# Kernel tuning notes

Measured on AMD Instinct MI355X. Metric: run time of the kernel, lower is better.

The kernel has to match this reference:

```python
import jax, jax.numpy as jnp
import numpy as np

B, S, H = 2, 2048, 1024
NH = 16
HD = H // NH


def setup_inputs() -> dict:
    key = jax.random.key(0)
    ks = jax.random.split(key, 5)
    X = jax.random.normal(ks[0], (B, S, H), dtype=jnp.float32)
    mask = jnp.ones((B, S), dtype=jnp.int32)
    W_Q = jax.random.normal(ks[1], (H, H), dtype=jnp.float32) * 0.02
    W_K = jax.random.normal(ks[2], (H, H), dtype=jnp.float32) * 0.02
    W_V = jax.random.normal(ks[3], (H, H), dtype=jnp.float32) * 0.02
    W_O = jax.random.normal(ks[4], (H, H), dtype=jnp.float32) * 0.02
    return {"X": X, "mask": mask, "W_Q": W_Q, "W_K": W_K, "W_V": W_V, "W_O": W_O}


def reference(X, mask, W_Q, W_K, W_V, W_O):
    b, s, h = X.shape
    scaling = HD ** -0.5
    # project and split heads: [b, nh, s, hd]
    Q = (X @ W_Q).reshape(b, s, NH, HD).transpose(0, 2, 1, 3)
    K = (X @ W_K).reshape(b, s, NH, HD).transpose(0, 2, 1, 3)
    V = (X @ W_V).reshape(b, s, NH, HD).transpose(0, 2, 1, 3)
    scores = jnp.einsum('bhqd,bhkd->bhqk', Q, K) * scaling
    scores = jnp.clip(scores, -10000.0, 10000.0)
    # 2D mask [b, s] -> broadcast as [b, 1, 1, s]; fill -inf where mask == 0
    m = mask[:, None, None, :]
    scores = jnp.where(m == 0, -jnp.inf, scores)
    attn = jax.nn.softmax(scores, axis=-1)
    # dropout is identity in eval / p=0
    context = jnp.einsum('bhqk,bhkd->bhqd', attn, V)
    context = context.transpose(0, 2, 1, 3).reshape(b, s, h)
    return context @ W_O
```

## Files before the change

### kernel.cpp

```cpp
#include <hip/hip_runtime.h>
#include <hip/hip_bf16.h>

#define S_LEN 2048
#define HDIM  1024
#define NHEADS 16
#define HD    64
#define QKV_STRIDE (S_LEN * 2 * HDIM)

typedef __attribute__((ext_vector_type(8))) short short8;
typedef __attribute__((ext_vector_type(4))) float float4v;

__device__ __forceinline__ unsigned short f2bf(float f) {
  return (unsigned short)((__builtin_bit_cast(unsigned int, f) + 0x8000u) >> 16);
}
__device__ __forceinline__ unsigned int pkbf(float a, float b) {
  unsigned int ua = __builtin_bit_cast(unsigned int, a) + 0x8000u;
  unsigned int ub = __builtin_bit_cast(unsigned int, b) + 0x8000u;
  return __builtin_amdgcn_perm(ub, ua, 0x07060302u);
}

__device__ __forceinline__ void async_copy16(const void* g, void* l) {
  __builtin_amdgcn_global_load_lds((__attribute__((address_space(1))) const void*)g,
                                   (__attribute__((address_space(3))) void*)l, 16, 0, 0);
}

__global__ void cast_x_kernel(const float* __restrict__ X, unsigned short* __restrict__ Xb) {
  int i = blockIdx.x * blockDim.x + threadIdx.x;
  float4 v = ((const float4*)X)[i];
  uint2 o;
  o.x = pkbf(v.x, v.y);
  o.y = pkbf(v.z, v.w);
  ((uint2*)Xb)[i] = o;
}

__global__ void trans_w_kernel(const float* __restrict__ W0, const float* __restrict__ W1,
                               const float* __restrict__ W2, const float* __restrict__ W3,
                               unsigned short* __restrict__ Wt) {
  __shared__ unsigned short tile[64][72];
  const float* W = (blockIdx.z == 0) ? W0 : (blockIdx.z == 1) ? W1 : (blockIdx.z == 2) ? W2 : W3;
  unsigned short* out = Wt + (size_t)blockIdx.z * HDIM * HDIM;
  int n0 = blockIdx.x * 64, k0 = blockIdx.y * 64;
  int t = threadIdx.x;
#pragma unroll
  for (int it = 0; it < 4; ++it) {
    int idx = it * 256 + t;
    int r  = idx >> 4;
    int c4 = (idx & 15) * 4;
    float4 v = *(const float4*)&W[(size_t)(k0 + r) * HDIM + n0 + c4];
    tile[c4 + 0][r] = f2bf(v.x);
    tile[c4 + 1][r] = f2bf(v.y);
    tile[c4 + 2][r] = f2bf(v.z);
    tile[c4 + 3][r] = f2bf(v.w);
  }
  __syncthreads();
#pragma unroll
  for (int it = 0; it < 4; ++it) {
    int idx = it * 256 + t;
    int r  = idx >> 4;
    int c4 = (idx & 15) * 4;
    ushort4 o;
    o.x = tile[r][c4 + 0]; o.y = tile[r][c4 + 1];
    o.z = tile[r][c4 + 2]; o.w = tile[r][c4 + 3];
    *(ushort4*)&out[(size_t)(n0 + r) * HDIM + k0 + c4] = o;
  }
}

__global__ __launch_bounds__(256, 3) void gemm128_kernel(
    const unsigned short* __restrict__ A,
    const unsigned short* __restrict__ B0, const unsigned short* __restrict__ B1,
    const unsigned short* __restrict__ B2,
    void* __restrict__ outp, int mode)
{
  __shared__ unsigned short sA[128 * 32];
  __shared__ unsigned short sB[128 * 32];
  const int z = blockIdx.z;
  const unsigned short* Bt = (z == 0) ? B0 : (z == 1) ? B1 : B2;
  const int m0 = blockIdx.x * 128;
  const int n0 = blockIdx.y * 128;
  const int t = threadIdx.x;
  const int lane = t & 63;
  const int w = t >> 6;
  const int wm = w & 1, wn = w >> 1;

  const int sr  = lane >> 2;
  const int scp = lane & 3;
  const int scl = scp ^ ((sr >> 1) & 3);
  const long ga0 = (long)(m0 + 16 * w + sr) * HDIM + scl * 8;
  const long ga1 = ga0 + 64l * HDIM;
  const long gb0 = (long)(n0 + 16 * w + sr) * HDIM + scl * 8;
  const long gb1 = gb0 + 64l * HDIM;
  unsigned short* lA0 = &sA[(16 * w) * 32];
  unsigned short* lA1 = &sA[(64 + 16 * w) * 32];
  unsigned short* lB0 = &sB[(16 * w) * 32];
  unsigned short* lB1 = &sB[(64 + 16 * w) * 32];

  const int fr = lane & 15;
  const int fq = lane >> 4;
  int offA[4], offB[4];
#pragma unroll
  for (int i = 0; i < 4; ++i) {
    int ra = wm * 64 + i * 16 + fr;
    offA[i] = ra * 32 + (fq ^ ((ra >> 1) & 3)) * 8;
    int rb = wn * 64 + i * 16 + fr;
    offB[i] = rb * 32 + (fq ^ ((rb >> 1) & 3)) * 8;
  }

  float4v acc[4][4] = {};

  for (int kk = 0; kk < HDIM; kk += 32) {
    __syncthreads();
    async_copy16(A + ga0 + kk, lA0);
    async_copy16(A + ga1 + kk, lA1);
    async_copy16(Bt + gb0 + kk, lB0);
    async_copy16(Bt + gb1 + kk, lB1);
    __syncthreads();
    short8 af[4], bf[4];
#pragma unroll
    for (int i = 0; i < 4; ++i) af[i] = *(const short8*)&sA[offA[i]];
#pragma unroll
    for (int i = 0; i < 4; ++i) bf[i] = *(const short8*)&sB[offB[i]];
#pragma unroll
    for (int mi = 0; mi < 4; ++mi)
#pragma unroll
      for (int ni = 0; ni < 4; ++ni)
        acc[mi][ni] = __builtin_amdgcn_mfma_f32_16x16x32_bf16(af[mi], bf[ni], acc[mi][ni], 0, 0, 0);
  }

  if (mode == 0) {
    float* out = (float*)outp;
#pragma unroll
    for (int mi = 0; mi < 4; ++mi)
#pragma unroll
      for (int ni = 0; ni < 4; ++ni)
#pragma unroll
        for (int rg = 0; rg < 4; ++rg) {
          int m = m0 + wm * 64 + mi * 16 + fq * 4 + rg;
          int n = n0 + wn * 64 + ni * 16 + fr;
          out[(size_t)m * HDIM + n] = acc[mi][ni][rg];
        }
  } else if (z != 1) {
    const float scl = (z == 0) ? 0.18033688011112042f : 1.0f;
    unsigned short* out = (unsigned short*)outp + (size_t)z * QKV_STRIDE;
#pragma unroll
    for (int mi = 0; mi < 4; ++mi)
#pragma unroll
      for (int ni = 0; ni < 4; ++ni) {
        int m = m0 + wm * 64 + mi * 16 + fq * 4;
        int n = n0 + wn * 64 + ni * 16 + fr;
        int b = m >> 11, s = m & 2047, hh = n >> 6, d = n & 63;
        uint2 pk;
        pk.x = pkbf(acc[mi][ni][0] * scl, acc[mi][ni][1] * scl);
        pk.y = pkbf(acc[mi][ni][2] * scl, acc[mi][ni][3] * scl);
        *(uint2*)&out[(((size_t)(b * NHEADS + hh)) * HD + d) * S_LEN + s] = pk;
      }
  } else {
    unsigned short* out = (unsigned short*)outp + (size_t)z * QKV_STRIDE;
#pragma unroll
    for (int mi = 0; mi < 4; ++mi)
#pragma unroll
      for (int ni = 0; ni < 4; ++ni)
#pragma unroll
        for (int rg = 0; rg < 4; ++rg) {
          int m = m0 + wm * 64 + mi * 16 + fq * 4 + rg;
          int n = n0 + wn * 64 + ni * 16 + fr;
          int b = m >> 11, s = m & 2047, hh = n >> 6, d = n & 63;
          out[(((size_t)(b * NHEADS + hh)) * S_LEN + s) * HD + d] = f2bf(acc[mi][ni][rg]);
        }
  }
}

__global__ __launch_bounds__(512, 4) void attn_kernel(
    const unsigned short* __restrict__ Qtp,
    const unsigned short* __restrict__ Kp,
    const unsigned short* __restrict__ Vtp,
    const int* __restrict__ mask,
    unsigned short* __restrict__ ctx)
{
  __shared__ __align__(16) char smem[65536];
  unsigned short* sK  = (unsigned short*)smem;
  unsigned short* sVt = (unsigned short*)(smem + 16384);
  unsigned short* sP0 = (unsigned short*)(smem + 32768);

  const int bh = blockIdx.y;
  const int b = bh >> 4;
  const int h = bh & 15;
  const size_t base = (size_t)bh * (S_LEN * HD);
  const int q0 = blockIdx.x * 128;
  const int t = threadIdx.x;
  const int lane = t & 63;
  const int w = t >> 6;
  const int qg = w >> 1;
  const int kh = w & 1;
  const int fr = lane & 15;
  const int fq = lane >> 4;
  unsigned short* sPw = sP0 + w * (32 * 64);

  short8 qfr[2][2];
#pragma unroll
  for (int q_ = 0; q_ < 2; ++q_)
#pragma unroll
    for (int ks = 0; ks < 2; ++ks)
#pragma unroll
      for (int j = 0; j < 8; ++j)
        qfr[q_][ks][j] = (short)Qtp[base + (size_t)(ks * 32 + fq * 8 + j) * S_LEN
                                    + (q0 + qg * 32 + q_ * 16 + fr)];

  float l_lane[2] = {0.f, 0.f};
  float4v o_acc[4][2] = {};

  const int kr = lane >> 3, kc = lane & 7;
  const int vr = lane >> 4, vc = lane & 15;
  const float NEG = -1e30f;

  for (int kv0 = 0; kv0 < S_LEN; kv0 += 128) {
    __syncthreads();
#pragma unroll
    for (int o = 0; o < 2; ++o) {
      int row0 = w * 16 + o * 8;
      async_copy16(Kp + base + (size_t)(kv0 + row0 + kr) * HD + ((kc ^ kr) * 8), &sK[row0 * HD]);
    }
#pragma unroll
    for (int o = 0; o < 2; ++o) {
      int d0 = w * 8 + o * 4;
      int d  = d0 + vr;
      async_copy16(Vtp + base + (size_t)d * S_LEN + kv0 + ((vc ^ (d & 15)) * 8), &sVt[d0 * 128]);
    }
    __syncthreads();

    float4v s_acc[4][2];
    const float4v zero4 = {0.f, 0.f, 0.f, 0.f};
#pragma unroll
    for (int kf = 0; kf < 4; ++kf) {
      int rk = kh * 64 + kf * 16 + fr;
      short8 k0 = *(const short8*)&sK[rk * HD + ((fq ^ (fr & 7)) * 8)];
      short8 k1 = *(const short8*)&sK[rk * HD + (((4 + fq) ^ (fr & 7)) * 8)];
#pragma unroll
      for (int q_ = 0; q_ < 2; ++q_) {
        float4v s = __builtin_amdgcn_mfma_f32_16x16x32_bf16(k0, qfr[q_][0], zero4, 0, 0, 0);
        s_acc[kf][q_] = __builtin_amdgcn_mfma_f32_16x16x32_bf16(k1, qfr[q_][1], s, 0, 0, 0);
      }
    }

    const int prow0 = fr * 64;
#pragma unroll
    for (int kf = 0; kf < 4; ++kf) {
      int4 mv = *(const int4*)&mask[b * S_LEN + kv0 + kh * 64 + kf * 16 + fq * 4];
#pragma unroll
      for (int q_ = 0; q_ < 2; ++q_) {
        float p0 = __builtin_amdgcn_exp2f(mv.x ? s_acc[kf][q_][0] : NEG);
        float p1 = __builtin_amdgcn_exp2f(mv.y ? s_acc[kf][q_][1] : NEG);
        float p2 = __builtin_amdgcn_exp2f(mv.z ? s_acc[kf][q_][2] : NEG);
        float p3 = __builtin_amdgcn_exp2f(mv.w ? s_acc[kf][q_][3] : NEG);
        l_lane[q_] += (p0 + p1) + (p2 + p3);
        uint2 pk;
        pk.x = pkbf(p0, p1);
        pk.y = pkbf(p2, p3);
        *(uint2*)&sPw[prow0 + q_ * 16 * 64 + (((kf * 4 + fq) ^ (fr & 14)) << 2)] = pk;
      }
    }

#pragma unroll
    for (int ks = 0; ks < 2; ++ks) {
      short8 pf[2], vf[4];
#pragma unroll
      for (int q_ = 0; q_ < 2; ++q_)
        pf[q_] = *(const short8*)&sPw[prow0 + q_ * 16 * 64 + (((ks * 8 + fq * 2) ^ (fr & 14)) << 2)];
#pragma unroll
      for (int df = 0; df < 4; ++df)
        vf[df] = *(const short8*)&sVt[(df * 16 + fr) * 128 + (((kh * 8 + ks * 4 + fq) ^ fr) << 3)];
#pragma unroll
      for (int df = 0; df < 4; ++df)
#pragma unroll
        for (int q_ = 0; q_ < 2; ++q_)
          o_acc[df][q_] = __builtin_amdgcn_mfma_f32_16x16x32_bf16(vf[df], pf[q_], o_acc[df][q_], 0, 0, 0);
    }
  }

#pragma unroll
  for (int q_ = 0; q_ < 2; ++q_) {
    l_lane[q_] += __shfl_xor(l_lane[q_], 16);
    l_lane[q_] += __shfl_xor(l_lane[q_], 32);
  }

  __syncthreads();
  float* red = (float*)smem;
  float* rec = red + (size_t)(qg * 64 + lane) * 34;
  if (kh) {
#pragma unroll
    for (int df = 0; df < 4; ++df)
#pragma unroll
      for (int q_ = 0; q_ < 2; ++q_) {
        int e = df * 2 + q_;
        *(float2*)&rec[4 * e]     = make_float2(o_acc[df][q_][0], o_acc[df][q_][1]);
        *(float2*)&rec[4 * e + 2] = make_float2(o_acc[df][q_][2], o_acc[df][q_][3]);
      }
    *(float2*)&rec[32] = make_float2(l_lane[0], l_lane[1]);
  }
  __syncthreads();
  if (!kh) {
#pragma unroll
    for (int df = 0; df < 4; ++df)
#pragma unroll
      for (int q_ = 0; q_ < 2; ++q_) {
        int e = df * 2 + q_;
        float2 a = *(float2*)&rec[4 * e];
        float2 c = *(float2*)&rec[4 * e + 2];
        o_acc[df][q_][0] += a.x; o_acc[df][q_][1] += a.y;
        o_acc[df][q_][2] += c.x; o_acc[df][q_][3] += c.y;
      }
    float2 lr = *(float2*)&rec[32];
    float inv_l[2];
    inv_l[0] = 1.0f / (l_lane[0] + lr.x);
    inv_l[1] = 1.0f / (l_lane[1] + lr.y);
#pragma unroll
    for (int q_ = 0; q_ < 2; ++q_) {
      size_t rowoff = ((size_t)(b * S_LEN + q0 + qg * 32 + q_ * 16 + fr)) * HDIM + h * HD;
#pragma unroll
      for (int df = 0; df < 4; ++df) {
        uint2 pk;
        pk.x = pkbf(o_acc[df][q_][0] * inv_l[q_], o_acc[df][q_][1] * inv_l[q_]);
        pk.y = pkbf(o_acc[df][q_][2] * inv_l[q_], o_acc[df][q_][3] * inv_l[q_]);
        *(uint2*)&ctx[rowoff + df * 16 + fq * 4] = pk;
      }
    }
  }
}

extern "C" void kernel_launch(void* const* d_in, const int* in_sizes, int n_in,
                              void* d_out, int out_size, void* d_ws, size_t ws_size,
                              hipStream_t stream) {
  const float* X  = (const float*)d_in[0];
  const int* mask = (const int*)d_in[1];
  const float* Wq = (const float*)d_in[2];
  const float* Wk = (const float*)d_in[3];
  const float* Wv = (const float*)d_in[4];
  const float* Wo = (const float*)d_in[5];
  float* out = (float*)d_out;

  char* ws = (char*)d_ws;
  unsigned short* Xb  = (unsigned short*)(ws);
  unsigned short* Wt  = (unsigned short*)(ws + (8u << 20));
  unsigned short* QKV = (unsigned short*)(ws + (16u << 20));
  unsigned short* CTX = (unsigned short*)(ws);

  cast_x_kernel<<<4096, 256, 0, stream>>>(X, Xb);
  trans_w_kernel<<<dim3(16, 16, 4), 256, 0, stream>>>(Wq, Wk, Wv, Wo, Wt);
  gemm128_kernel<<<dim3(32, 8, 3), 256, 0, stream>>>(
      Xb, Wt, Wt + (1u << 20), Wt + (2u << 20), QKV, 1);
  attn_kernel<<<dim3(16, 32), 512, 0, stream>>>(
      QKV, QKV + QKV_STRIDE, QKV + 2 * (size_t)QKV_STRIDE, mask, CTX);
  gemm128_kernel<<<dim3(32, 8, 1), 256, 0, stream>>>(
      CTX, Wt + (3u << 20), Wt + (3u << 20), Wt + (3u << 20), out, 0);
}
```

Measured before the change: 197.7 us.

## Double-buffer K/V tiles with 64-key steps and prefetch next tile

```diff
diff --git a/kernel.cpp b/kernel.cpp
--- a/kernel.cpp
+++ b/kernel.cpp
@@ -169,6 +169,17 @@
   }
 }
 
+__device__ __forceinline__ void stage_tile(char* smem, const unsigned short* Kp,
+    const unsigned short* Vtp, size_t base, int tile, int w, int kr, int kc) {
+  const int kv = tile * 64;
+  char* bufb = smem + (tile & 1) * 16384;
+  unsigned short* dK = (unsigned short*)bufb + (w * 8) * 64;
+  async_copy16(Kp + base + (size_t)(kv + w * 8 + kr) * HD + ((kc ^ kr) * 8), dK);
+  unsigned short* dV = (unsigned short*)(bufb + 8192) + (w * 8) * 64;
+  const int d = w * 8 + kr;
+  async_copy16(Vtp + base + (size_t)d * S_LEN + kv + ((kc ^ kr) * 8), dV);
+}
+
 __global__ __launch_bounds__(512, 4) void attn_kernel(
     const unsigned short* __restrict__ Qtp,
     const unsigned short* __restrict__ Kp,
@@ -176,10 +187,7 @@
     const int* __restrict__ mask,
     unsigned short* __restrict__ ctx)
 {
-  __shared__ __align__(16) char smem[65536];
-  unsigned short* sK  = (unsigned short*)smem;
-  unsigned short* sVt = (unsigned short*)(smem + 16384);
-  unsigned short* sP0 = (unsigned short*)(smem + 32768);
+  __shared__ __align__(16) char smem[53248];
 
   const int bh = blockIdx.y;
   const int b = bh >> 4;
@@ -193,7 +201,8 @@
   const int kh = w & 1;
   const int fr = lane & 15;
   const int fq = lane >> 4;
-  unsigned short* sPw = sP0 + w * (32 * 64);
+  const int kr = lane >> 3, kc = lane & 7;
+  unsigned short* sPw = (unsigned short*)(smem + 32768) + w * (32 * 40);
 
   short8 qfr[2][2];
 #pragma unroll
@@ -207,33 +216,27 @@
 
   float l_lane[2] = {0.f, 0.f};
   float4v o_acc[4][2] = {};
-
-  const int kr = lane >> 3, kc = lane & 7;
-  const int vr = lane >> 4, vc = lane & 15;
   const float NEG = -1e30f;
-
-  for (int kv0 = 0; kv0 < S_LEN; kv0 += 128) {
+  const float4v zero4 = {0.f, 0.f, 0.f, 0.f};
+
+  stage_tile(smem, Kp, Vtp, base, 0, w, kr, kc);
+
+#pragma unroll 2
+  for (int it = 0; it < 32; ++it) {
     __syncthreads();
-#pragma unroll
-    for (int o = 0; o < 2; ++o) {
-      int row0 = w * 16 + o * 8;
-      async_copy16(Kp + base + (size_t)(kv0 + row0 + kr) * HD + ((kc ^ kr) * 8), &sK[row0 * HD]);
-    }
-#pragma unroll
-    for (int o = 0; o < 2; ++o) {
-      int d0 = w * 8 + o * 4;
-      int d  = d0 + vr;
-      async_copy16(Vtp + base + (size_t)d * S_LEN + kv0 + ((vc ^ (d & 15)) * 8), &sVt[d0 * 128]);
-    }
-    __syncthreads();
-
-    float4v s_acc[4][2];
-    const float4v zero4 = {0.f, 0.f, 0.f, 0.f};
-#pragma unroll
-    for (int kf = 0; kf < 4; ++kf) {
-      int rk = kh * 64 + kf * 16 + fr;
-      short8 k0 = *(const short8*)&sK[rk * HD + ((fq ^ (fr & 7)) * 8)];
-      short8 k1 = *(const short8*)&sK[rk * HD + (((4 + fq) ^ (fr & 7)) * 8)];
+    if (it < 31)
+      stage_tile(smem, Kp, Vtp, base, it + 1, w, kr, kc);
+
+    const unsigned short* sKb  = (const unsigned short*)(smem + (it & 1) * 16384);
+    const unsigned short* sVtb = (const unsigned short*)(smem + (it & 1) * 16384 + 8192);
+    const int kv0 = it * 64;
+
+    float4v s_acc[2][2];
+#pragma unroll
+    for (int kf = 0; kf < 2; ++kf) {
+      int rk = kh * 32 + kf * 16 + fr;
+      short8 k0 = *(const short8*)&sKb[rk * 64 + ((fq ^ (rk & 7)) * 8)];
+      short8 k1 = *(const short8*)&sKb[rk * 64 + (((4 + fq) ^ (rk & 7)) * 8)];
 #pragma unroll
       for (int q_ = 0; q_ < 2; ++q_) {
         float4v s = __builtin_amdgcn_mfma_f32_16x16x32_bf16(k0, qfr[q_][0], zero4, 0, 0, 0);
@@ -241,10 +244,9 @@
       }
     }
 
-    const int prow0 = fr * 64;
-#pragma unroll
-    for (int kf = 0; kf < 4; ++kf) {
-      int4 mv = *(const int4*)&mask[b * S_LEN + kv0 + kh * 64 + kf * 16 + fq * 4];
+#pragma unroll
+    for (int kf = 0; kf < 2; ++kf) {
+      int4 mv = *(const int4*)&mask[b * S_LEN + kv0 + kh * 32 + kf * 16 + fq * 4];
 #pragma unroll
       for (int q_ = 0; q_ < 2; ++q_) {
         float p0 = __builtin_amdgcn_exp2f(mv.x ? s_acc[kf][q_][0] : NEG);
@@ -255,25 +257,24 @@
         uint2 pk;
         pk.x = pkbf(p0, p1);
         pk.y = pkbf(p2, p3);
-        *(uint2*)&sPw[prow0 + q_ * 16 * 64 + (((kf * 4 + fq) ^ (fr & 14)) << 2)] = pk;
+        *(uint2*)&sPw[(q_ * 16 + fr) * 40 + (kf * 4 + fq) * 4] = pk;
       }
     }
 
-#pragma unroll
-    for (int ks = 0; ks < 2; ++ks) {
-      short8 pf[2], vf[4];
+    short8 pf[2], vf[4];
+#pragma unroll
+    for (int q_ = 0; q_ < 2; ++q_)
+      pf[q_] = *(const short8*)&sPw[(q_ * 16 + fr) * 40 + fq * 8];
+#pragma unroll
+    for (int df = 0; df < 4; ++df) {
+      int rv = df * 16 + fr;
+      vf[df] = *(const short8*)&sVtb[rv * 64 + (((kh * 4 + fq) ^ (fr & 7)) * 8)];
+    }
+#pragma unroll
+    for (int df = 0; df < 4; ++df)
 #pragma unroll
       for (int q_ = 0; q_ < 2; ++q_)
-        pf[q_] = *(const short8*)&sPw[prow0 + q_ * 16 * 64 + (((ks * 8 + fq * 2) ^ (fr & 14)) << 2)];
-#pragma unroll
-      for (int df = 0; df < 4; ++df)
-        vf[df] = *(const short8*)&sVt[(df * 16 + fr) * 128 + (((kh * 8 + ks * 4 + fq) ^ fr) << 3)];
-#pragma unroll
-      for (int df = 0; df < 4; ++df)
-#pragma unroll
-        for (int q_ = 0; q_ < 2; ++q_)
-          o_acc[df][q_] = __builtin_amdgcn_mfma_f32_16x16x32_bf16(vf[df], pf[q_], o_acc[df][q_], 0, 0, 0);
-    }
+        o_acc[df][q_] = __builtin_amdgcn_mfma_f32_16x16x32_bf16(vf[df], pf[q_], o_acc[df][q_], 0, 0, 0);
   }
 
 #pragma unroll
```

Result: faster. 192.1 us (-2.8%).
